# Performance work log

Hardware: AMD Instinct MI355X
Metric: run time of the kernel (lower is better)

## Reference

```python
import jax, jax.numpy as jnp
import numpy as np

B, N, D, H, K = 4, 256, 128, 8, 16

def setup_inputs() -> dict:
    key = jax.random.key(0)
    ks = jax.random.split(key, 6)
    h = jax.random.normal(ks[0], (B, N, D), jnp.float32)
    e_att = jax.random.normal(ks[1], (B, N, N, H, K), jnp.float32)
    e_val = jax.random.normal(ks[2], (B, N, N, H, K), jnp.float32)
    mask = jnp.ones((B, N), jnp.float32)
    scale = 1.0 / np.sqrt(D).astype(np.float32)
    Wq = jax.random.normal(ks[3], (D, H * K), jnp.float32) * scale
    Wk = jax.random.normal(ks[4], (D, H * K), jnp.float32) * scale
    Wv = jax.random.normal(ks[5], (D, H * K), jnp.float32) * scale
    return {"h": h, "e_att": e_att, "e_val": e_val, "mask": mask, "Wq": Wq, "Wk": Wk, "Wv": Wv}

def reference(h, e_att, e_val, mask, Wq, Wk, Wv):
    b, n, _ = h.shape
    Q = (h @ Wq).reshape(b, n, H, K)
    Kh = (h @ Wk).reshape(b, n, H, K) * (float(K) ** -0.5)
    V = (h @ Wv).reshape(b, n, H, K)
    # (b,i,j,h) dot-product scores, broadcast over k, plus per-edge bias
    scores = jnp.einsum('bihk,bjhk->bijh', Q, Kh)[..., None] + e_att
    scores = jnp.exp(jnp.clip(scores, -5.0, 5.0))
    attn_mask = mask[:, :, None, None, None] * mask[:, None, :, None, None]
    scores = scores * attn_mask
    softmax_denom = jnp.maximum(scores.sum(axis=2), 1e-6)  # (b,i,h,k)
    scores = scores * attn_mask  # dropout p=0 -> identity on mask
    out = jnp.einsum('bijhk,bjhk->bihk', scores, V)
    out = out + (scores * e_val).sum(axis=2)
    out = out / softmax_denom
    return out.reshape(b, n, H * K)
```

## Files before the change

kernel.cpp:

```cpp
#include <hip/hip_runtime.h>
#include <hip/hip_bf16.h>

#define Bb 4
#define Nn 256
#define Dd 128
#define Hh 8
#define Kk 16
#define HK 128
#define BN 1024

__global__ __launch_bounds__(128) void qkv_kernel(
    const float* __restrict__ h,
    const float* __restrict__ Wq,
    const float* __restrict__ Wk,
    const float* __restrict__ Wv,
    float* __restrict__ Qw, float* __restrict__ Kw, float* __restrict__ Vw)
{
    __shared__ float hrows[8][Dd];
    const int rb = blockIdx.x;
    const int t  = threadIdx.x;
    #pragma unroll
    for (int r = 0; r < 8; ++r)
        hrows[r][t] = h[(size_t)(rb * 8 + r) * Dd + t];
    __syncthreads();

    float aq[8], ak[8], av[8];
    #pragma unroll
    for (int r = 0; r < 8; ++r) { aq[r] = 0.f; ak[r] = 0.f; av[r] = 0.f; }

    for (int d = 0; d < Dd; ++d) {
        const float wq = Wq[d * HK + t];
        const float wk = Wk[d * HK + t];
        const float wv = Wv[d * HK + t];
        #pragma unroll
        for (int r = 0; r < 8; ++r) {
            const float hv = hrows[r][d];
            aq[r] = fmaf(hv, wq, aq[r]);
            ak[r] = fmaf(hv, wk, ak[r]);
            av[r] = fmaf(hv, wv, av[r]);
        }
    }
    #pragma unroll
    for (int r = 0; r < 8; ++r) {
        const size_t o = (size_t)(rb * 8 + r) * HK + t;
        Qw[o] = aq[r];
        Kw[o] = ak[r] * 0.25f;
        Vw[o] = av[r];
    }
}

__global__ __launch_bounds__(256) void qk_kernel(
    const float* __restrict__ Qw,
    const float* __restrict__ Kw,
    float* __restrict__ qkg)
{
    __shared__ float qrow[HK];
    const int t  = threadIdx.x;
    const int bi = blockIdx.x;
    const int b  = bi >> 8;

    if (t < HK) qrow[t] = Qw[(size_t)bi * HK + t];
    __syncthreads();

    #pragma unroll
    for (int p = 0; p < 8; ++p) {
        const int idx = p * 256 + t;
        const int j   = idx >> 3;
        const int hh  = idx & 7;
        const float4* kp = (const float4*)(Kw + (size_t)(b * Nn + j) * HK + hh * Kk);
        const float4 k0 = kp[0], k1 = kp[1], k2 = kp[2], k3 = kp[3];
        const float* qp = qrow + hh * Kk;
        float acc = 0.f;
        acc = fmaf(qp[0],  k0.x, acc); acc = fmaf(qp[1],  k0.y, acc);
        acc = fmaf(qp[2],  k0.z, acc); acc = fmaf(qp[3],  k0.w, acc);
        acc = fmaf(qp[4],  k1.x, acc); acc = fmaf(qp[5],  k1.y, acc);
        acc = fmaf(qp[6],  k1.z, acc); acc = fmaf(qp[7],  k1.w, acc);
        acc = fmaf(qp[8],  k2.x, acc); acc = fmaf(qp[9],  k2.y, acc);
        acc = fmaf(qp[10], k2.z, acc); acc = fmaf(qp[11], k2.w, acc);
        acc = fmaf(qp[12], k3.x, acc); acc = fmaf(qp[13], k3.y, acc);
        acc = fmaf(qp[14], k3.z, acc); acc = fmaf(qp[15], k3.w, acc);
        qkg[(size_t)bi * 2048 + idx] = acc;
    }
}

__global__ __launch_bounds__(512) void attn_kernel(
    const float* __restrict__ e_att,
    const float* __restrict__ e_val,
    const float* __restrict__ mask,
    const float* __restrict__ qkg,
    const float* __restrict__ Vw,
    float* __restrict__ out)
{
    __shared__ float qk_s[2048];
    __shared__ float mrow[Nn];
    __shared__ float red[3 * 16 * HK];

    const int t  = threadIdx.x;
    const int bi = blockIdx.x;
    const int b  = bi >> 8;

    ((float4*)qk_s)[t] = ((const float4*)(qkg + (size_t)bi * 2048))[t];
    if (t < Nn) mrow[t] = mask[b * Nn + t];
    __syncthreads();

    const float maski = mrow[bi & 255];

    const int q32  = t & 31;
    const int joff = t >> 5;
    const int hk4  = q32 * 4;
    const int hh   = q32 >> 2;

    float acc_d[4] = {0,0,0,0}, acc_v[4] = {0,0,0,0}, acc_e[4] = {0,0,0,0};
    const size_t slice = (size_t)bi * (Nn * HK);

    #pragma unroll 4
    for (int jb = 0; jb < Nn; jb += 16) {
        const int j = jb + joff;
        const size_t eoff = slice + (size_t)j * HK + hk4;
        const float4 ea = *(const float4*)(e_att + eoff);
        const float4 ev = *(const float4*)(e_val + eoff);
        const float4 v4 = *(const float4*)(Vw + (size_t)(b * Nn + j) * HK + hk4);

        const float qk = qk_s[(j << 3) + hh];
        const float m  = maski * mrow[j];
        const float m2 = m * m;

        const float eaf[4] = {ea.x, ea.y, ea.z, ea.w};
        const float evf[4] = {ev.x, ev.y, ev.z, ev.w};
        const float vv[4]  = {v4.x, v4.y, v4.z, v4.w};

        #pragma unroll
        for (int l = 0; l < 4; ++l) {
            float x = qk + eaf[l];
            x = fminf(fmaxf(x, -5.f), 5.f);
            const float e = __expf(x);
            acc_d[l] = fmaf(e, m, acc_d[l]);
            const float s2 = e * m2;
            acc_v[l] = fmaf(s2, vv[l], acc_v[l]);
            acc_e[l] = fmaf(s2, evf[l], acc_e[l]);
        }
    }
    __syncthreads();

    #pragma unroll
    for (int l = 0; l < 4; ++l) {
        red[0 * 2048 + joff * HK + hk4 + l] = acc_d[l];
        red[1 * 2048 + joff * HK + hk4 + l] = acc_v[l];
        red[2 * 2048 + joff * HK + hk4 + l] = acc_e[l];
    }
    __syncthreads();

    if (t < HK) {
        float D = 0.f, OV = 0.f, OE = 0.f;
        #pragma unroll
        for (int p = 0; p < 16; ++p) {
            D  += red[0 * 2048 + p * HK + t];
            OV += red[1 * 2048 + p * HK + t];
            OE += red[2 * 2048 + p * HK + t];
        }
        out[(size_t)bi * HK + t] = (OV + OE) / fmaxf(D, 1e-6f);
    }
}

extern "C" void kernel_launch(void* const* d_in, const int* in_sizes, int n_in,
                              void* d_out, int out_size, void* d_ws, size_t ws_size,
                              hipStream_t stream) {
    const float* h     = (const float*)d_in[0];
    const float* e_att = (const float*)d_in[1];
    const float* e_val = (const float*)d_in[2];
    const float* mask  = (const float*)d_in[3];
    const float* Wq    = (const float*)d_in[4];
    const float* Wk    = (const float*)d_in[5];
    const float* Wv    = (const float*)d_in[6];
    float* out = (float*)d_out;

    float* Qw  = (float*)d_ws;
    float* Kw  = Qw + (size_t)BN * HK;
    float* Vw  = Kw + (size_t)BN * HK;
    float* qkg = Vw + (size_t)BN * HK;

    qkv_kernel<<<128, 128, 0, stream>>>(h, Wq, Wk, Wv, Qw, Kw, Vw);
    qk_kernel<<<BN, 256, 0, stream>>>(Qw, Kw, qkg);
    attn_kernel<<<BN, 512, 0, stream>>>(e_att, e_val, mask, qkg, Vw, out);
}
```

Before: 74.41 us.

## Fuse QK score computation into attention kernel and software-pipeline edge loads

Removes the separate qk_kernel and its 8 MB qkg intermediate. Each attention block now computes its own row of Q·K scores into padded shared memory (stride 9, to avoid bank conflicts). The main j loop is fully unrolled with double-buffered register prefetch of e_att, e_val and V, so loads overlap with the exp/FMA work. The cost is extra shared memory and register pressure, plus the K-row dot products recomputed inside each block.

New measurement: 73.62 us. Within noise of the previous version (-1.1%).

```diff
diff --git a/kernel.cpp b/kernel.cpp
--- a/kernel.cpp
+++ b/kernel.cpp
@@ -49,61 +49,55 @@
     }
 }
 
-__global__ __launch_bounds__(256) void qk_kernel(
-    const float* __restrict__ Qw,
-    const float* __restrict__ Kw,
-    float* __restrict__ qkg)
-{
-    __shared__ float qrow[HK];
-    const int t  = threadIdx.x;
-    const int bi = blockIdx.x;
-    const int b  = bi >> 8;
-
-    if (t < HK) qrow[t] = Qw[(size_t)bi * HK + t];
-    __syncthreads();
-
-    #pragma unroll
-    for (int p = 0; p < 8; ++p) {
-        const int idx = p * 256 + t;
-        const int j   = idx >> 3;
-        const int hh  = idx & 7;
-        const float4* kp = (const float4*)(Kw + (size_t)(b * Nn + j) * HK + hh * Kk);
-        const float4 k0 = kp[0], k1 = kp[1], k2 = kp[2], k3 = kp[3];
-        const float* qp = qrow + hh * Kk;
-        float acc = 0.f;
-        acc = fmaf(qp[0],  k0.x, acc); acc = fmaf(qp[1],  k0.y, acc);
-        acc = fmaf(qp[2],  k0.z, acc); acc = fmaf(qp[3],  k0.w, acc);
-        acc = fmaf(qp[4],  k1.x, acc); acc = fmaf(qp[5],  k1.y, acc);
-        acc = fmaf(qp[6],  k1.z, acc); acc = fmaf(qp[7],  k1.w, acc);
-        acc = fmaf(qp[8],  k2.x, acc); acc = fmaf(qp[9],  k2.y, acc);
-        acc = fmaf(qp[10], k2.z, acc); acc = fmaf(qp[11], k2.w, acc);
-        acc = fmaf(qp[12], k3.x, acc); acc = fmaf(qp[13], k3.y, acc);
-        acc = fmaf(qp[14], k3.z, acc); acc = fmaf(qp[15], k3.w, acc);
-        qkg[(size_t)bi * 2048 + idx] = acc;
-    }
-}
+#define QKP 9
 
 __global__ __launch_bounds__(512) void attn_kernel(
     const float* __restrict__ e_att,
     const float* __restrict__ e_val,
     const float* __restrict__ mask,
-    const float* __restrict__ qkg,
+    const float* __restrict__ Qw,
+    const float* __restrict__ Kw,
     const float* __restrict__ Vw,
     float* __restrict__ out)
 {
-    __shared__ float qk_s[2048];
+    __shared__ float qrow[HK];
     __shared__ float mrow[Nn];
+    __shared__ float qk_s[Nn * QKP];
     __shared__ float red[3 * 16 * HK];
 
     const int t  = threadIdx.x;
     const int bi = blockIdx.x;
     const int b  = bi >> 8;
 
-    ((float4*)qk_s)[t] = ((const float4*)(qkg + (size_t)bi * 2048))[t];
+    if (t < HK) qrow[t] = Qw[(size_t)bi * HK + t];
     if (t < Nn) mrow[t] = mask[b * Nn + t];
     __syncthreads();
 
     const float maski = mrow[bi & 255];
+
+    {
+        const int j    = t >> 1;
+        const int half = t & 1;
+        const float4* kp = (const float4*)(Kw + (size_t)(b * Nn + j) * HK + half * 64);
+        const float*  qp = qrow + half * 64;
+        #pragma unroll
+        for (int hl = 0; hl < 4; ++hl) {
+            const float4 k0 = kp[hl * 4 + 0], k1 = kp[hl * 4 + 1];
+            const float4 k2 = kp[hl * 4 + 2], k3 = kp[hl * 4 + 3];
+            const float* q = qp + hl * Kk;
+            float acc = 0.f;
+            acc = fmaf(q[0],  k0.x, acc); acc = fmaf(q[1],  k0.y, acc);
+            acc = fmaf(q[2],  k0.z, acc); acc = fmaf(q[3],  k0.w, acc);
+            acc = fmaf(q[4],  k1.x, acc); acc = fmaf(q[5],  k1.y, acc);
+            acc = fmaf(q[6],  k1.z, acc); acc = fmaf(q[7],  k1.w, acc);
+            acc = fmaf(q[8],  k2.x, acc); acc = fmaf(q[9],  k2.y, acc);
+            acc = fmaf(q[10], k2.z, acc); acc = fmaf(q[11], k2.w, acc);
+            acc = fmaf(q[12], k3.x, acc); acc = fmaf(q[13], k3.y, acc);
+            acc = fmaf(q[14], k3.z, acc); acc = fmaf(q[15], k3.w, acc);
+            qk_s[j * QKP + half * 4 + hl] = acc;
+        }
+    }
+    __syncthreads();
 
     const int q32  = t & 31;
     const int joff = t >> 5;
@@ -112,34 +106,54 @@
 
     float acc_d[4] = {0,0,0,0}, acc_v[4] = {0,0,0,0}, acc_e[4] = {0,0,0,0};
     const size_t slice = (size_t)bi * (Nn * HK);
+    const float* vbase = Vw + (size_t)(b * Nn) * HK;
 
-    #pragma unroll 4
-    for (int jb = 0; jb < Nn; jb += 16) {
-        const int j = jb + joff;
-        const size_t eoff = slice + (size_t)j * HK + hk4;
-        const float4 ea = *(const float4*)(e_att + eoff);
-        const float4 ev = *(const float4*)(e_val + eoff);
-        const float4 v4 = *(const float4*)(Vw + (size_t)(b * Nn + j) * HK + hk4);
+#define LOADSET(EA, EV, VV, JB) do {                                         \
+        const int j_ = (JB) + joff;                                          \
+        const size_t eo_ = slice + (size_t)j_ * HK + hk4;                    \
+        EA = *(const float4*)(e_att + eo_);                                  \
+        EV = *(const float4*)(e_val + eo_);                                  \
+        VV = *(const float4*)(vbase + (size_t)j_ * HK + hk4);                \
+    } while (0)
 
-        const float qk = qk_s[(j << 3) + hh];
-        const float m  = maski * mrow[j];
-        const float m2 = m * m;
+#define COMPUTE(EA, EV, VV, JB) do {                                         \
+        const int j_ = (JB) + joff;                                          \
+        const float qk_ = qk_s[j_ * QKP + hh];                               \
+        const float m_  = maski * mrow[j_];                                  \
+        const float m2_ = m_ * m_;                                           \
+        const float eaf_[4] = {EA.x, EA.y, EA.z, EA.w};                      \
+        const float evf_[4] = {EV.x, EV.y, EV.z, EV.w};                      \
+        const float vvf_[4] = {VV.x, VV.y, VV.z, VV.w};                      \
+        _Pragma("unroll")                                                    \
+        for (int l = 0; l < 4; ++l) {                                        \
+            float x_ = qk_ + eaf_[l];                                        \
+            x_ = fminf(fmaxf(x_, -5.f), 5.f);                                \
+            const float e_ = __expf(x_);                                     \
+            acc_d[l] = fmaf(e_, m_, acc_d[l]);                               \
+            const float s2_ = e_ * m2_;                                      \
+            acc_v[l] = fmaf(s2_, vvf_[l], acc_v[l]);                         \
+            acc_e[l] = fmaf(s2_, evf_[l], acc_e[l]);                         \
+        }                                                                    \
+    } while (0)
 
-        const float eaf[4] = {ea.x, ea.y, ea.z, ea.w};
-        const float evf[4] = {ev.x, ev.y, ev.z, ev.w};
-        const float vv[4]  = {v4.x, v4.y, v4.z, v4.w};
+    float4 eaA, evA, vvA, eaB, evB, vvB;
+    LOADSET(eaA, evA, vvA, 0);
+    LOADSET(eaB, evB, vvB, 16);
 
-        #pragma unroll
-        for (int l = 0; l < 4; ++l) {
-            float x = qk + eaf[l];
-            x = fminf(fmaxf(x, -5.f), 5.f);
-            const float e = __expf(x);
-            acc_d[l] = fmaf(e, m, acc_d[l]);
-            const float s2 = e * m2;
-            acc_v[l] = fmaf(s2, vv[l], acc_v[l]);
-            acc_e[l] = fmaf(s2, evf[l], acc_e[l]);
-        }
+    #pragma unroll
+    for (int k = 0; k < 7; ++k) {
+        const int jb = k * 32;
+        COMPUTE(eaA, evA, vvA, jb);
+        LOADSET(eaA, evA, vvA, jb + 32);
+        COMPUTE(eaB, evB, vvB, jb + 16);
+        LOADSET(eaB, evB, vvB, jb + 48);
     }
+    COMPUTE(eaA, evA, vvA, 224);
+    COMPUTE(eaB, evB, vvB, 240);
+
+#undef LOADSET
+#undef COMPUTE
+
     __syncthreads();
 
     #pragma unroll
@@ -177,9 +191,7 @@
     float* Qw  = (float*)d_ws;
     float* Kw  = Qw + (size_t)BN * HK;
     float* Vw  = Kw + (size_t)BN * HK;
-    float* qkg = Vw + (size_t)BN * HK;
 
     qkv_kernel<<<128, 128, 0, stream>>>(h, Wq, Wk, Wv, Qw, Kw, Vw);
-    qk_kernel<<<BN, 256, 0, stream>>>(Qw, Kw, qkg);
-    attn_kernel<<<BN, 512, 0, stream>>>(e_att, e_val, mask, qkg, Vw, out);
+    attn_kernel<<<BN, 512, 0, stream>>>(e_att, e_val, mask, Qw, Kw, Vw, out);
 }
```
